# Performance work log

Measured on AMD Instinct MI355X. Metric: run time of the kernel, lower is better.

The kernel has to match this reference:

```python
import jax, jax.numpy as jnp
import numpy as np

B, T, D, U = 64, 2048, 256, 256

def setup_inputs() -> dict:
    key = jax.random.key(0)
    ks = jax.random.split(key, 8)
    return {
        "query": jax.random.normal(ks[0], (B, D), dtype=jnp.float32),
        "values": jax.random.normal(ks[1], (B, T, D), dtype=jnp.float32),
        "W1_w": jax.random.normal(ks[2], (D, U), dtype=jnp.float32) * 0.05,
        "W1_b": jnp.zeros((U,), dtype=jnp.float32),
        "W2_w": jax.random.normal(ks[3], (D, U), dtype=jnp.float32) * 0.05,
        "W2_b": jnp.zeros((U,), dtype=jnp.float32),
        "V_w": jax.random.normal(ks[4], (U, 1), dtype=jnp.float32) * 0.05,
        "V_b": jnp.zeros((1,), dtype=jnp.float32),
    }

def reference(query, values, W1_w, W1_b, W2_w, W2_b, V_w, V_b):
    # query: [B, D] -> [B, 1, U]
    q_proj = (query @ W1_w + W1_b)[:, None, :]
    # values: [B, T, D] -> [B, T, U]
    v_proj = jnp.einsum('btd,du->btu', values, W2_w) + W2_b
    # score: [B, T, 1]
    score = jnp.tanh(q_proj + v_proj) @ V_w + V_b
    attention_weights = jax.nn.softmax(score, axis=1)  # over time axis
    context_vector = jnp.sum(attention_weights * values, axis=1)  # [B, D]
    return (context_vector, attention_weights)
```

## Files before the change

### kernel.cpp

```cpp
#include <hip/hip_runtime.h>
#include <hip/hip_fp16.h>

#define B_ 64
#define T_ 2048
#define D_ 256
#define U_ 256
#define BT 256
#define NT (BT / 16)
#define TC (T_ / BT)

typedef _Float16 half8  __attribute__((ext_vector_type(8)));
typedef float    floatx4 __attribute__((ext_vector_type(4)));

typedef const __attribute__((address_space(1))) void cg_void;
typedef __attribute__((address_space(3))) void       ls_void;

__global__ void prep_kernel(const float* __restrict__ query,
                            const float* __restrict__ W1_w,
                            const float* __restrict__ W1_b,
                            const float* __restrict__ W2_w,
                            const float* __restrict__ W2_b,
                            float* __restrict__ qb,
                            _Float16* __restrict__ w2t) {
    __shared__ float sh[32 * 33];
    if (blockIdx.x < 64) {
        const int b = blockIdx.x;
        const int u = threadIdx.x;
        sh[u] = query[b * D_ + u];
        __syncthreads();
        float acc = W1_b[u] + W2_b[u];
#pragma unroll 8
        for (int d = 0; d < D_; ++d)
            acc += sh[d] * W1_w[d * U_ + u];
        qb[b * U_ + u] = acc;
    } else {
        const int bid = blockIdx.x - 64;
        const int tu = bid & 7;
        const int td = bid >> 3;
        const int c  = threadIdx.x & 31;
        const int r0 = threadIdx.x >> 5;
        float* tile = sh;
#pragma unroll
        for (int i = 0; i < 4; ++i) {
            int r = r0 + i * 8;
            tile[r * 33 + c] = W2_w[(td * 32 + r) * U_ + tu * 32 + c];
        }
        __syncthreads();
#pragma unroll
        for (int i = 0; i < 4; ++i) {
            int r = r0 + i * 8;
            w2t[(tu * 32 + r) * D_ + td * 32 + c] = (_Float16)tile[c * 33 + r];
        }
    }
}

__launch_bounds__(512, 4)
__global__ void score_ctx_kernel(const float* __restrict__ values,
                                 const _Float16* __restrict__ w2t,
                                 const float* __restrict__ qb,
                                 const float* __restrict__ V_w,
                                 float* __restrict__ wexp,
                                 float* __restrict__ pctx,
                                 float* __restrict__ pl) {
    __shared__ __align__(16) float vbuf[2][16 * D_];
    __shared__ __align__(16) float s_part[2][16][8];
    __shared__ float csum[512];
    __shared__ float lsum[2];

    const int b     = blockIdx.y;
    const int chunk = blockIdx.x;
    const int tid   = threadIdx.x;
    const int wave  = tid >> 6;
    const int lane  = tid & 63;
    const int n16   = lane & 15;
    const int quad  = lane >> 4;
    const int u0    = wave * 32;

    half8 bfrag[2][8];
#pragma unroll
    for (int ut = 0; ut < 2; ++ut) {
        const int u = u0 + ut * 16 + n16;
#pragma unroll
        for (int k = 0; k < 8; ++k)
            bfrag[ut][k] = *(const half8*)(w2t + u * D_ + k * 32 + quad * 8);
    }
    float qbv[2], vwv[2];
#pragma unroll
    for (int ut = 0; ut < 2; ++ut) {
        const int u = u0 + ut * 16 + n16;
        qbv[ut] = qb[b * U_ + u];
        vwv[ut] = V_w[u];
    }

    const float* vbase = values + (size_t)b * T_ * D_ + (size_t)chunk * BT * D_;

    auto stage = [&](int tile, int bi) {
        const float* src = vbase + tile * 16 * D_;
#pragma unroll
        for (int i = 0; i < 2; ++i) {
            const int r = wave * 2 + i;
            const float* g = src + r * D_ + ((lane ^ (r & 7)) << 2);
            float* l = &vbuf[bi][r * D_];
            __builtin_amdgcn_global_load_lds((cg_void*)g, (ls_void*)l, 16, 0, 0);
        }
    };

    stage(0, 0);

    float c     = 0.f;
    float l_run = 0.f;
    const int half = tid >> 8;
    const int dd   = tid & 255;
    const int ccx  = dd >> 2, lo = dd & 3;

    float* wout = wexp + b * T_ + chunk * BT;

    for (int t = 0; t < NT; ++t) {
        __syncthreads();
        if (t + 1 < NT) stage(t + 1, (t + 1) & 1);

        floatx4 acc[2] = {};
        const float* rowbase = &vbuf[t & 1][n16 * D_];
        const int swz = n16 & 7;
#pragma unroll
        for (int k = 0; k < 8; ++k) {
            const int c0 = k * 8 + quad * 2;
            floatx4 q0 = *(const floatx4*)(rowbase + (((c0    ) ^ swz) << 2));
            floatx4 q1 = *(const floatx4*)(rowbase + (((c0 + 1) ^ swz) << 2));
            half8 a;
            a[0] = (_Float16)q0.x; a[1] = (_Float16)q0.y;
            a[2] = (_Float16)q0.z; a[3] = (_Float16)q0.w;
            a[4] = (_Float16)q1.x; a[5] = (_Float16)q1.y;
            a[6] = (_Float16)q1.z; a[7] = (_Float16)q1.w;
#pragma unroll
            for (int ut = 0; ut < 2; ++ut)
                acc[ut] = __builtin_amdgcn_mfma_f32_16x16x32_f16(a, bfrag[ut][k], acc[ut], 0, 0, 0);
        }

        float part[4];
#pragma unroll
        for (int r = 0; r < 4; ++r) {
            float s = 0.f;
#pragma unroll
            for (int ut = 0; ut < 2; ++ut) {
                float x  = acc[ut][r] + qbv[ut];
                float e  = __expf(2.f * x);
                float th = 1.f - __fdividef(2.f, e + 1.f);
                s += th * vwv[ut];
            }
            part[r] = s;
        }
#pragma unroll
        for (int m = 1; m < 16; m <<= 1)
#pragma unroll
            for (int r = 0; r < 4; ++r)
                part[r] += __shfl_xor(part[r], m, 16);
        if (n16 == 0)
#pragma unroll
            for (int r = 0; r < 4; ++r)
                s_part[t & 1][quad * 4 + r][wave] = part[r];

        __syncthreads();

#pragma unroll
        for (int j = 0; j < 8; ++j) {
            const int r = half * 8 + j;
            floatx4 p0 = *(const floatx4*)&s_part[t & 1][r][0];
            floatx4 p1 = *(const floatx4*)&s_part[t & 1][r][4];
            float s = ((p0.x + p0.y) + (p0.z + p0.w)) + ((p1.x + p1.y) + (p1.z + p1.w));
            float w = __expf(s);
            l_run += w;
            c += w * vbuf[t & 1][r * D_ + ((ccx ^ (r & 7)) << 2) + lo];
            if (dd == j) wout[t * 16 + r] = w;
        }
    }

    __syncthreads();
    csum[tid] = c;
    if (dd == 0) lsum[half] = l_run;
    __syncthreads();
    if (tid < 256) pctx[(b * TC + chunk) * D_ + tid] = csum[tid] + csum[tid + 256];
    if (tid == 0)  pl[b * TC + chunk] = lsum[0] + lsum[1];
}

__global__ void finalize_kernel(const float* __restrict__ pctx,
                                const float* __restrict__ pl,
                                const float* __restrict__ wexp,
                                float* __restrict__ ctx,
                                float* __restrict__ attn) {
    const int b = blockIdx.x, tid = threadIdx.x;
    float L = 0.f;
#pragma unroll
    for (int i = 0; i < TC; ++i) L += pl[b * TC + i];
    const float invL = 1.f / L;
    float s = 0.f;
#pragma unroll
    for (int i = 0; i < TC; ++i) s += pctx[(b * TC + i) * D_ + tid];
    ctx[b * D_ + tid] = s * invL;
#pragma unroll
    for (int j = 0; j < T_ / 256; ++j) {
        const int t = j * 256 + tid;
        attn[b * T_ + t] = wexp[b * T_ + t] * invL;
    }
}

extern "C" void kernel_launch(void* const* d_in, const int* in_sizes, int n_in,
                              void* d_out, int out_size, void* d_ws, size_t ws_size,
                              hipStream_t stream) {
    const float* query  = (const float*)d_in[0];
    const float* values = (const float*)d_in[1];
    const float* W1_w   = (const float*)d_in[2];
    const float* W1_b   = (const float*)d_in[3];
    const float* W2_w   = (const float*)d_in[4];
    const float* W2_b   = (const float*)d_in[5];
    const float* V_w    = (const float*)d_in[6];

    float* out  = (float*)d_out;
    float* ctx  = out;
    float* attn = out + B_ * D_;

    char* ws = (char*)d_ws;
    float*    qb   = (float*)ws;
    _Float16* w2t  = (_Float16*)(ws + (64 << 10));
    float*    wexp = (float*)(ws + (192 << 10));
    float*    pctx = (float*)(ws + (704 << 10));
    float*    pl   = (float*)(ws + (1216 << 10));

    prep_kernel     <<<dim3(128),     dim3(256), 0, stream>>>(query, W1_w, W1_b, W2_w, W2_b, qb, w2t);
    score_ctx_kernel<<<dim3(TC, B_),  dim3(512), 0, stream>>>(values, w2t, qb, V_w, wexp, pctx, pl);
    finalize_kernel <<<dim3(B_),      dim3(256), 0, stream>>>(pctx, pl, wexp, ctx, attn);
}
```

Measured before the change: 288.5 us.

## Split score and context into separate kernels with fp16 LDS A-tiles

Replaces the fused score/context kernel with a score kernel that processes 128-row blocks. It stages values as fp16 into swizzled LDS tiles of 32 rows using register prefetch, and issues 2x2 MFMA tiles per wave. The context sum now runs in a separate kernel that re-reads values from global memory, weighted by the stored exponentials. This removes the per-tile weighted-sum work and the fp32 LDS staging from the MFMA loop, and pins the B fragments into AGPRs. The cost is reading the 134MB values tensor twice plus an extra launch.

```diff
diff --git a/kernel.cpp b/kernel.cpp
--- a/kernel.cpp
+++ b/kernel.cpp
@@ -5,15 +5,12 @@
 #define T_ 2048
 #define D_ 256
 #define U_ 256
-#define BT 256
-#define NT (BT / 16)
-#define TC (T_ / BT)
+#define RB 128
+#define NTB (T_ / RB)
+#define CC 8
 
 typedef _Float16 half8  __attribute__((ext_vector_type(8)));
 typedef float    floatx4 __attribute__((ext_vector_type(4)));
-
-typedef const __attribute__((address_space(1))) void cg_void;
-typedef __attribute__((address_space(3))) void       ls_void;
 
 __global__ void prep_kernel(const float* __restrict__ query,
                             const float* __restrict__ W1_w,
@@ -55,132 +52,167 @@
 }
 
 __launch_bounds__(512, 4)
-__global__ void score_ctx_kernel(const float* __restrict__ values,
-                                 const _Float16* __restrict__ w2t,
-                                 const float* __restrict__ qb,
-                                 const float* __restrict__ V_w,
-                                 float* __restrict__ wexp,
-                                 float* __restrict__ pctx,
-                                 float* __restrict__ pl) {
-    __shared__ __align__(16) float vbuf[2][16 * D_];
-    __shared__ __align__(16) float s_part[2][16][8];
-    __shared__ float csum[512];
-    __shared__ float lsum[2];
-
-    const int b     = blockIdx.y;
-    const int chunk = blockIdx.x;
-    const int tid   = threadIdx.x;
-    const int wave  = tid >> 6;
-    const int lane  = tid & 63;
-    const int n16   = lane & 15;
-    const int quad  = lane >> 4;
-    const int u0    = wave * 32;
+__global__ void score_kernel(const float* __restrict__ values,
+                             const _Float16* __restrict__ w2t,
+                             const float* __restrict__ qb,
+                             const float* __restrict__ V_w,
+                             float* __restrict__ wexp,
+                             float* __restrict__ pl) {
+    __shared__ __align__(16) _Float16 Atile[2][32 * 256];
+    __shared__ __align__(16) float s_part[RB][8];
+    __shared__ float red2[2];
+
+    const int b    = blockIdx.y;
+    const int tb   = blockIdx.x;
+    const int tid  = threadIdx.x;
+    const int wave = tid >> 6;
+    const int lane = tid & 63;
+    const int n16  = lane & 15;
+    const int quad = lane >> 4;
+    const int u0   = wave * 32;
 
     half8 bfrag[2][8];
 #pragma unroll
-    for (int ut = 0; ut < 2; ++ut) {
-        const int u = u0 + ut * 16 + n16;
-#pragma unroll
-        for (int k = 0; k < 8; ++k)
-            bfrag[ut][k] = *(const half8*)(w2t + u * D_ + k * 32 + quad * 8);
+    for (int nt = 0; nt < 2; ++nt) {
+        const int u = u0 + nt * 16 + n16;
+#pragma unroll
+        for (int ks = 0; ks < 8; ++ks) {
+            bfrag[nt][ks] = *(const half8*)(w2t + u * D_ + ks * 32 + quad * 8);
+            asm volatile("" : "+a"(bfrag[nt][ks]));
+        }
     }
     float qbv[2], vwv[2];
 #pragma unroll
-    for (int ut = 0; ut < 2; ++ut) {
-        const int u = u0 + ut * 16 + n16;
-        qbv[ut] = qb[b * U_ + u];
-        vwv[ut] = V_w[u];
-    }
-
-    const float* vbase = values + (size_t)b * T_ * D_ + (size_t)chunk * BT * D_;
-
-    auto stage = [&](int tile, int bi) {
-        const float* src = vbase + tile * 16 * D_;
-#pragma unroll
-        for (int i = 0; i < 2; ++i) {
-            const int r = wave * 2 + i;
-            const float* g = src + r * D_ + ((lane ^ (r & 7)) << 2);
-            float* l = &vbuf[bi][r * D_];
-            __builtin_amdgcn_global_load_lds((cg_void*)g, (ls_void*)l, 16, 0, 0);
-        }
-    };
-
-    stage(0, 0);
-
-    float c     = 0.f;
-    float l_run = 0.f;
-    const int half = tid >> 8;
-    const int dd   = tid & 255;
-    const int ccx  = dd >> 2, lo = dd & 3;
-
-    float* wout = wexp + b * T_ + chunk * BT;
-
-    for (int t = 0; t < NT; ++t) {
+    for (int nt = 0; nt < 2; ++nt) {
+        const int u = u0 + nt * 16 + n16;
+        qbv[nt] = qb[b * U_ + u];
+        vwv[nt] = V_w[u];
+    }
+
+    const int rl = tid >> 4;
+    const int pp = tid & 15;
+    const float* srow = values + ((size_t)b * T_ + (size_t)tb * RB + rl) * D_ + pp * 16;
+
+    floatx4 sv[4];
+#pragma unroll
+    for (int i = 0; i < 4; ++i) sv[i] = *(const floatx4*)(srow + i * 4);
+#pragma unroll
+    for (int i = 0; i < 2; ++i) {
+        half8 h;
+        h[0] = (_Float16)sv[2*i].x; h[1] = (_Float16)sv[2*i].y;
+        h[2] = (_Float16)sv[2*i].z; h[3] = (_Float16)sv[2*i].w;
+        h[4] = (_Float16)sv[2*i+1].x; h[5] = (_Float16)sv[2*i+1].y;
+        h[6] = (_Float16)sv[2*i+1].z; h[7] = (_Float16)sv[2*i+1].w;
+        const int cp = (2 * pp + i) ^ (rl & 7);
+        *(half8*)(&Atile[0][rl * 256 + cp * 8]) = h;
+    }
+
+    for (int rnd = 0; rnd < 4; ++rnd) {
         __syncthreads();
-        if (t + 1 < NT) stage(t + 1, (t + 1) & 1);
-
-        floatx4 acc[2] = {};
-        const float* rowbase = &vbuf[t & 1][n16 * D_];
-        const int swz = n16 & 7;
-#pragma unroll
-        for (int k = 0; k < 8; ++k) {
-            const int c0 = k * 8 + quad * 2;
-            floatx4 q0 = *(const floatx4*)(rowbase + (((c0    ) ^ swz) << 2));
-            floatx4 q1 = *(const floatx4*)(rowbase + (((c0 + 1) ^ swz) << 2));
-            half8 a;
-            a[0] = (_Float16)q0.x; a[1] = (_Float16)q0.y;
-            a[2] = (_Float16)q0.z; a[3] = (_Float16)q0.w;
-            a[4] = (_Float16)q1.x; a[5] = (_Float16)q1.y;
-            a[6] = (_Float16)q1.z; a[7] = (_Float16)q1.w;
-#pragma unroll
-            for (int ut = 0; ut < 2; ++ut)
-                acc[ut] = __builtin_amdgcn_mfma_f32_16x16x32_f16(a, bfrag[ut][k], acc[ut], 0, 0, 0);
-        }
-
-        float part[4];
-#pragma unroll
-        for (int r = 0; r < 4; ++r) {
-            float s = 0.f;
-#pragma unroll
-            for (int ut = 0; ut < 2; ++ut) {
-                float x  = acc[ut][r] + qbv[ut];
-                float e  = __expf(2.f * x);
-                float th = 1.f - __fdividef(2.f, e + 1.f);
-                s += th * vwv[ut];
+        if (rnd < 3) {
+            const float* s2 = srow + (size_t)(rnd + 1) * 32 * D_;
+#pragma unroll
+            for (int i = 0; i < 4; ++i) sv[i] = *(const floatx4*)(s2 + i * 4);
+        }
+
+        floatx4 acc[2][2] = {};
+#pragma unroll
+        for (int ks = 0; ks < 8; ++ks) {
+#pragma unroll
+            for (int mt = 0; mt < 2; ++mt) {
+                const int rr = mt * 16 + n16;
+                const int cp = (ks * 4 + quad) ^ (n16 & 7);
+                half8 a = *(const half8*)(&Atile[rnd & 1][rr * 256 + cp * 8]);
+#pragma unroll
+                for (int nt = 0; nt < 2; ++nt)
+                    acc[mt][nt] = __builtin_amdgcn_mfma_f32_16x16x32_f16(a, bfrag[nt][ks], acc[mt][nt], 0, 0, 0);
             }
-            part[r] = s;
-        }
+        }
+
+        float rs[2][4];
+#pragma unroll
+        for (int mt = 0; mt < 2; ++mt)
+#pragma unroll
+            for (int r4 = 0; r4 < 4; ++r4) {
+                float s = 0.f;
+#pragma unroll
+                for (int nt = 0; nt < 2; ++nt) {
+                    float x  = acc[mt][nt][r4] + qbv[nt];
+                    float e  = __expf(2.f * x);
+                    float th = 1.f - __fdividef(2.f, e + 1.f);
+                    s += th * vwv[nt];
+                }
+                rs[mt][r4] = s;
+            }
 #pragma unroll
         for (int m = 1; m < 16; m <<= 1)
 #pragma unroll
-            for (int r = 0; r < 4; ++r)
-                part[r] += __shfl_xor(part[r], m, 16);
+            for (int mt = 0; mt < 2; ++mt)
+#pragma unroll
+                for (int r4 = 0; r4 < 4; ++r4)
+                    rs[mt][r4] += __shfl_xor(rs[mt][r4], m, 16);
         if (n16 == 0)
 #pragma unroll
-            for (int r = 0; r < 4; ++r)
-                s_part[t & 1][quad * 4 + r][wave] = part[r];
-
-        __syncthreads();
-
-#pragma unroll
-        for (int j = 0; j < 8; ++j) {
-            const int r = half * 8 + j;
-            floatx4 p0 = *(const floatx4*)&s_part[t & 1][r][0];
-            floatx4 p1 = *(const floatx4*)&s_part[t & 1][r][4];
-            float s = ((p0.x + p0.y) + (p0.z + p0.w)) + ((p1.x + p1.y) + (p1.z + p1.w));
-            float w = __expf(s);
-            l_run += w;
-            c += w * vbuf[t & 1][r * D_ + ((ccx ^ (r & 7)) << 2) + lo];
-            if (dd == j) wout[t * 16 + r] = w;
-        }
-    }
-
-    __syncthreads();
-    csum[tid] = c;
-    if (dd == 0) lsum[half] = l_run;
-    __syncthreads();
-    if (tid < 256) pctx[(b * TC + chunk) * D_ + tid] = csum[tid] + csum[tid + 256];
-    if (tid == 0)  pl[b * TC + chunk] = lsum[0] + lsum[1];
+            for (int mt = 0; mt < 2; ++mt)
+#pragma unroll
+                for (int r4 = 0; r4 < 4; ++r4)
+                    s_part[rnd * 32 + mt * 16 + quad * 4 + r4][wave] = rs[mt][r4];
+
+        if (rnd < 3) {
+#pragma unroll
+            for (int i = 0; i < 2; ++i) {
+                half8 h;
+                h[0] = (_Float16)sv[2*i].x; h[1] = (_Float16)sv[2*i].y;
+                h[2] = (_Float16)sv[2*i].z; h[3] = (_Float16)sv[2*i].w;
+                h[4] = (_Float16)sv[2*i+1].x; h[5] = (_Float16)sv[2*i+1].y;
+                h[6] = (_Float16)sv[2*i+1].z; h[7] = (_Float16)sv[2*i+1].w;
+                const int cp = (2 * pp + i) ^ (rl & 7);
+                *(half8*)(&Atile[(rnd + 1) & 1][rl * 256 + cp * 8]) = h;
+            }
+        }
+    }
+
+    __syncthreads();
+    if (tid < RB) {
+        floatx4 p0 = *(const floatx4*)&s_part[tid][0];
+        floatx4 p1 = *(const floatx4*)&s_part[tid][4];
+        float s = ((p0.x + p0.y) + (p0.z + p0.w)) + ((p1.x + p1.y) + (p1.z + p1.w));
+        float w = __expf(s);
+        wexp[b * T_ + tb * RB + tid] = w;
+        float ls = w;
+#pragma unroll
+        for (int m = 1; m < 64; m <<= 1) ls += __shfl_xor(ls, m, 64);
+        if (lane == 0) red2[wave] = ls;
+    }
+    __syncthreads();
+    if (tid == 0) pl[b * NTB + tb] = red2[0] + red2[1];
+}
+
+__global__ void context_kernel(const float* __restrict__ values,
+                               const float* __restrict__ wexp,
+                               float* __restrict__ pctx) {
+    __shared__ float w[256];
+    __shared__ floatx4 part[256];
+    const int b  = blockIdx.y;
+    const int ch = blockIdx.x;
+    const int tid = threadIdx.x;
+    w[tid] = wexp[b * T_ + ch * 256 + tid];
+    __syncthreads();
+    const int r = tid >> 6;
+    const int c = tid & 63;
+    const float* vb = values + ((size_t)b * T_ + (size_t)ch * 256) * D_;
+    floatx4 acc = {0.f, 0.f, 0.f, 0.f};
+#pragma unroll 4
+    for (int i = 0; i < 64; ++i) {
+        const int t = i * 4 + r;
+        acc += *(const floatx4*)(vb + t * D_ + c * 4) * w[t];
+    }
+    part[tid] = acc;
+    __syncthreads();
+    if (tid < 64) {
+        floatx4 s = part[tid] + part[tid + 64] + part[tid + 128] + part[tid + 192];
+        *(floatx4*)(pctx + ((size_t)b * CC + ch) * D_ + tid * 4) = s;
+    }
 }
 
 __global__ void finalize_kernel(const float* __restrict__ pctx,
@@ -191,11 +223,11 @@
     const int b = blockIdx.x, tid = threadIdx.x;
     float L = 0.f;
 #pragma unroll
-    for (int i = 0; i < TC; ++i) L += pl[b * TC + i];
+    for (int i = 0; i < NTB; ++i) L += pl[b * NTB + i];
     const float invL = 1.f / L;
     float s = 0.f;
 #pragma unroll
-    for (int i = 0; i < TC; ++i) s += pctx[(b * TC + i) * D_ + tid];
+    for (int i = 0; i < CC; ++i) s += pctx[(b * CC + i) * D_ + tid];
     ctx[b * D_ + tid] = s * invL;
 #pragma unroll
     for (int j = 0; j < T_ / 256; ++j) {
@@ -226,7 +258,8 @@
     float*    pctx = (float*)(ws + (704 << 10));
     float*    pl   = (float*)(ws + (1216 << 10));
 
-    prep_kernel     <<<dim3(128),     dim3(256), 0, stream>>>(query, W1_w, W1_b, W2_w, W2_b, qb, w2t);
-    score_ctx_kernel<<<dim3(TC, B_),  dim3(512), 0, stream>>>(values, w2t, qb, V_w, wexp, pctx, pl);
-    finalize_kernel <<<dim3(B_),      dim3(256), 0, stream>>>(pctx, pl, wexp, ctx, attn);
-}
+    prep_kernel    <<<dim3(128),      dim3(256), 0, stream>>>(query, W1_w, W1_b, W2_w, W2_b, qb, w2t);
+    score_kernel   <<<dim3(NTB, B_),  dim3(512), 0, stream>>>(values, w2t, qb, V_w, wexp, pl);
+    context_kernel <<<dim3(CC, B_),   dim3(256), 0, stream>>>(values, wexp, pctx);
+    finalize_kernel<<<dim3(B_),       dim3(256), 0, stream>>>(pctx, pl, wexp, ctx, attn);
+}
```

Measured after the change: 286.0 us. No clear change (-0.9%).
